# Kernel tuning notes

Measured on AMD Instinct MI355X. Metric: run time of the kernel, lower is better.

The kernel has to match this reference:

```python
import jax, jax.numpy as jnp
import numpy as np

N_NODES = 100000


def _gcn_norm(edge_index, num_nodes):
    # PyG GCNConv default: add self-loops, symmetric normalization
    src, dst = edge_index[0], edge_index[1]
    loop = jnp.arange(num_nodes, dtype=src.dtype)
    src = jnp.concatenate([src, loop])
    dst = jnp.concatenate([dst, loop])
    deg = jax.ops.segment_sum(jnp.ones_like(dst, dtype=jnp.float32), dst,
                              num_segments=num_nodes)
    dinv = jnp.where(deg > 0, jax.lax.rsqrt(deg), 0.0)
    norm = dinv[src] * dinv[dst]  # [E + N]
    return src, dst, norm


def _gcn_conv(x, W, b, src, dst, norm, num_nodes):
    h = x @ W                                   # [N, out] linear first (PyG)
    msg = h[src] * norm[:, None]                # gather + scale  [E+N, out]
    out = jax.ops.segment_sum(msg, dst, num_segments=num_nodes)  # scatter-add
    return out + b


def setup_inputs() -> dict:
    key = jax.random.key(0)
    ks = jax.random.split(key, 5)
    x = jax.random.normal(ks[0], (N_NODES, 3), dtype=jnp.float32)
    edge_index = jax.random.randint(ks[1], (2, 1600000), 0, N_NODES, dtype=jnp.int64)
    # Glorot-ish weights, zero bias (PyG defaults)
    W1 = jax.random.normal(ks[2], (3, 64), dtype=jnp.float32) * (1.0 / np.sqrt(3))
    W2 = jax.random.normal(ks[3], (64, 64), dtype=jnp.float32) * (1.0 / np.sqrt(64))
    W3 = jax.random.normal(ks[4], (64, 3), dtype=jnp.float32) * (1.0 / np.sqrt(64))
    b1 = jnp.zeros((64,), jnp.float32)
    b2 = jnp.zeros((64,), jnp.float32)
    b3 = jnp.zeros((3,), jnp.float32)
    return {"x": x, "edge_index": edge_index, "W1": W1, "b1": b1,
            "W2": W2, "b2": b2, "W3": W3, "b3": b3}


def reference(x, edge_index, W1, b1, W2, b2, W3, b3):
    n = x.shape[0]
    src, dst, norm = _gcn_norm(edge_index, n)  # same graph for every layer
    h = jax.nn.relu(_gcn_conv(x, W1, b1, src, dst, norm, n))
    h = jax.nn.relu(_gcn_conv(h, W2, b2, src, dst, norm, n))
    return _gcn_conv(h, W3, b3, src, dst, norm, n)
```

## Files before the change

### kernel.cpp

```cpp
#include <hip/hip_runtime.h>

#define TPB 256
#define NB 391
#define CH 4096
#define BS 4736


__device__ __forceinline__ unsigned bpack(float a, float b) {
    unsigned ua = __float_as_uint(a), ub = __float_as_uint(b);
    ua = (ua + 0x7fffu + ((ua >> 16) & 1u)) >> 16;
    ub = (ub + 0x7fffu + ((ub >> 16) & 1u)) >> 16;
    return ua | (ub << 16);
}
__device__ __forceinline__ float blo(unsigned u) { return __uint_as_float(u << 16); }
__device__ __forceinline__ float bhi(unsigned u) { return __uint_as_float(u & 0xffff0000u); }


__global__ __launch_bounds__(TPB) void k_placeA(const int* __restrict__ src,
                                                const int* __restrict__ dst,
                                                unsigned* __restrict__ gcur,
                                                unsigned* __restrict__ bkt, int E) {
    __shared__ unsigned val[CH];
    __shared__ unsigned dstS[CH];
    __shared__ unsigned short bid[CH];
    __shared__ unsigned cnt[512], loff[512], lcur[512], basev[512];
    __shared__ unsigned tsum[TPB];
    int t = threadIdx.x;
    int c0 = blockIdx.x * CH;
    int n = E - c0; if (n > CH) n = CH;

    for (int b = t; b < 512; b += TPB) { cnt[b] = 0; lcur[b] = 0; }
    __syncthreads();
    for (int i = t; i < n; i += TPB) {
        unsigned d = (unsigned)dst[c0 + i];
        dstS[i] = d;
        atomicAdd(&cnt[d >> 8], 1u);
    }
    __syncthreads();
    for (int b = t; b < NB; b += TPB)
        basev[b] = cnt[b] ? atomicAdd(&gcur[b], cnt[b]) : 0u;
    unsigned a0 = cnt[2 * t], a1 = cnt[2 * t + 1];
    tsum[t] = a0 + a1;
    __syncthreads();
#pragma unroll
    for (int o = 1; o < TPB; o <<= 1) {
        unsigned v = (t >= o) ? tsum[t - o] : 0u;
        __syncthreads();
        tsum[t] += v;
        __syncthreads();
    }
    unsigned ex = tsum[t] - (a0 + a1);
    loff[2 * t] = ex; loff[2 * t + 1] = ex + a0;
    __syncthreads();
    for (int i = t; i < n; i += TPB) {
        unsigned s = (unsigned)src[c0 + i];
        unsigned d = dstS[i];
        unsigned b = d >> 8;
        unsigned r = atomicAdd(&lcur[b], 1u);
        unsigned slot = loff[b] + r;
        val[slot] = s | ((d & 255u) << 20);
        bid[slot] = (unsigned short)b;
    }
    __syncthreads();
    for (int i = t; i < n; i += TPB) {
        unsigned b = bid[i];
        bkt[(size_t)b * BS + basev[b] + ((unsigned)i - loff[b])] = val[i];
    }
}


__global__ __launch_bounds__(512) void k_fineS(const unsigned* __restrict__ bkt,
                                               const unsigned* __restrict__ gcur,
                                               const float* __restrict__ x,
                                               int2* __restrict__ rp2,
                                               int* __restrict__ ssrc,
                                               float* __restrict__ dinv,
                                               float4* __restrict__ xs4, int N) {
    __shared__ unsigned bins[4096];
    __shared__ unsigned tsum[512];
    __shared__ unsigned degS[256];
    __shared__ unsigned bs[BS];
    int t = threadIdx.x, b = blockIdx.x;
    for (int i = t; i < 4096; i += 512) bins[i] = 0;
    __syncthreads();
    int p0 = b * BS;
    int n = (int)gcur[b];
    for (int i = t; i < n; i += 512) {
        unsigned u = bkt[p0 + i];
        bs[i] = u;
        unsigned bin = ((u >> 20) << 4) | ((u & 0xFFFFFu) >> 13);
        atomicAdd(&bins[bin], 1u);
    }
    __syncthreads();
    unsigned s[8], pre[8];
#pragma unroll
    for (int i = 0; i < 8; ++i) s[i] = bins[8 * t + i];
    if (t < 256) {
        unsigned d = 0;
#pragma unroll
        for (int i = 0; i < 16; ++i) d += bins[(t << 4) + i];
        degS[t] = d;
    }
    unsigned tot = 0;
#pragma unroll
    for (int i = 0; i < 8; ++i) { pre[i] = tot; tot += s[i]; }
    tsum[t] = tot;
    __syncthreads();
#pragma unroll
    for (int o = 1; o < 512; o <<= 1) {
        unsigned v = (t >= o) ? tsum[t - o] : 0u;
        __syncthreads();
        tsum[t] += v;
        __syncthreads();
    }
    unsigned ex = tsum[t] - tot;
#pragma unroll
    for (int i = 0; i < 8; ++i) bins[8 * t + i] = ex + pre[i];
    __syncthreads();
    if (t < 256) {
        int node = (b << 8) + t;
        if (node < N) {
            unsigned c = degS[t];
            int beg = p0 + (int)bins[t << 4];
            rp2[node] = make_int2(beg, beg + (int)c);
            float dv = rsqrtf((float)(c + 1u));
            dinv[node] = dv;
            float4 xv;
            xv.x = x[node * 3 + 0] * dv;
            xv.y = x[node * 3 + 1] * dv;
            xv.z = x[node * 3 + 2] * dv;
            xv.w = 0.f;
            xs4[node] = xv;
        }
    }
    __syncthreads();
    for (int i = t; i < n; i += 512) {
        unsigned u = bs[i];
        unsigned bin = ((u >> 20) << 4) | ((u & 0xFFFFFu) >> 13);
        unsigned r = atomicAdd(&bins[bin], 1u);
        ssrc[p0 + (int)r] = (int)(u & 0xFFFFFu);
    }
}


__global__ __launch_bounds__(TPB) void k_l1q(const float* __restrict__ xs4,
                                             const int2* __restrict__ rp2,
                                             const int* __restrict__ ssrc,
                                             const float* __restrict__ dinv,
                                             const float* __restrict__ W1,
                                             const float* __restrict__ b1,
                                             const float* __restrict__ W2,
                                             uint4* __restrict__ gb, int N) {
    __shared__ unsigned Ws2[2048];
    for (int i = threadIdx.x; i < 2048; i += TPB)
        Ws2[i] = bpack(W2[2 * i], W2[2 * i + 1]);
    __syncthreads();
    int tid = blockIdx.x * TPB + threadIdx.x;
    int node = tid >> 2, c = tid & 3;
    if (node >= N) return;
    int2 r = rp2[node];
    float acc = xs4[tid];
    int j = r.x;
    for (; j + 3 < r.y; j += 4) {
        int s0 = ssrc[j], s1 = ssrc[j+1], s2 = ssrc[j+2], s3 = ssrc[j+3];
        acc += (xs4[(s0 << 2) + c] + xs4[(s1 << 2) + c])
             + (xs4[(s2 << 2) + c] + xs4[(s3 << 2) + c]);
    }
    for (; j < r.y; ++j) acc += xs4[(ssrc[j] << 2) + c];
    float dv = dinv[node];
    acc *= dv;
    int base = (threadIdx.x & 63) & ~3;
    float q0 = __shfl(acc, base + 0, 64);
    float q1 = __shfl(acc, base + 1, 64);
    float q2 = __shfl(acc, base + 2, 64);

    float o[16];
#pragma unroll
    for (int i = 0; i < 16; ++i) o[i] = 0.f;
    const int cofs8 = c << 3;
    for (int kb = 0; kb < 16; ++kb) {
        int k0 = __builtin_amdgcn_readfirstlane(kb) << 2;
        const float* W1k = W1 + k0;
        const float* b1k = b1 + k0;
        float h[4];
        h[0] = fmaxf(fmaf(q0, W1k[0], fmaf(q1, W1k[64], fmaf(q2, W1k[128], b1k[0]))), 0.f);
        h[1] = fmaxf(fmaf(q0, W1k[1], fmaf(q1, W1k[65], fmaf(q2, W1k[129], b1k[1]))), 0.f);
        h[2] = fmaxf(fmaf(q0, W1k[2], fmaf(q1, W1k[66], fmaf(q2, W1k[130], b1k[2]))), 0.f);
        h[3] = fmaxf(fmaf(q0, W1k[3], fmaf(q1, W1k[67], fmaf(q2, W1k[131], b1k[3]))), 0.f);
#pragma unroll
        for (int kk = 0; kk < 4; ++kk) {
            const uint4* Wp = (const uint4*)(Ws2 + ((k0 + kk) << 5) + cofs8);
            uint4 wA = Wp[0];
            uint4 wB = Wp[1];
            float hv = h[kk];
            o[0]  = fmaf(hv, blo(wA.x), o[0]);  o[1]  = fmaf(hv, bhi(wA.x), o[1]);
            o[2]  = fmaf(hv, blo(wA.y), o[2]);  o[3]  = fmaf(hv, bhi(wA.y), o[3]);
            o[4]  = fmaf(hv, blo(wA.z), o[4]);  o[5]  = fmaf(hv, bhi(wA.z), o[5]);
            o[6]  = fmaf(hv, blo(wA.w), o[6]);  o[7]  = fmaf(hv, bhi(wA.w), o[7]);
            o[8]  = fmaf(hv, blo(wB.x), o[8]);  o[9]  = fmaf(hv, bhi(wB.x), o[9]);
            o[10] = fmaf(hv, blo(wB.y), o[10]); o[11] = fmaf(hv, bhi(wB.y), o[11]);
            o[12] = fmaf(hv, blo(wB.z), o[12]); o[13] = fmaf(hv, bhi(wB.z), o[13]);
            o[14] = fmaf(hv, blo(wB.w), o[14]); o[15] = fmaf(hv, bhi(wB.w), o[15]);
        }
    }
    uint4 v0, v1;
    v0.x = bpack(o[0] * dv,  o[1] * dv);
    v0.y = bpack(o[2] * dv,  o[3] * dv);
    v0.z = bpack(o[4] * dv,  o[5] * dv);
    v0.w = bpack(o[6] * dv,  o[7] * dv);
    v1.x = bpack(o[8] * dv,  o[9] * dv);
    v1.y = bpack(o[10] * dv, o[11] * dv);
    v1.z = bpack(o[12] * dv, o[13] * dv);
    v1.w = bpack(o[14] * dv, o[15] * dv);
    uint4* gp = gb + ((size_t)node << 3) + (c << 1);
    gp[0] = v0;
    gp[1] = v1;
}


__global__ __launch_bounds__(TPB) void k_p2fb(const uint4* __restrict__ gb,
                                              const int2* __restrict__ rp2,
                                              const int* __restrict__ ssrc,
                                              const float* __restrict__ dinv,
                                              const float* __restrict__ b2,
                                              const float* __restrict__ W3,
                                              float* __restrict__ q4, int N) {
    int tid = blockIdx.x * TPB + threadIdx.x;
    int node = tid >> 3, q = tid & 7;
    if (node >= N) return;
    int2 r = rp2[node];
    int beg = r.x, end = r.y;
    float a[8];
    {
        uint4 u = gb[((size_t)node << 3) + q];
        a[0] = blo(u.x); a[1] = bhi(u.x);
        a[2] = blo(u.y); a[3] = bhi(u.y);
        a[4] = blo(u.z); a[5] = bhi(u.z);
        a[6] = blo(u.w); a[7] = bhi(u.w);
    }
    int j = beg;
    for (; j + 3 < end; j += 4) {
        int s0 = ssrc[j], s1 = ssrc[j+1], s2 = ssrc[j+2], s3 = ssrc[j+3];
        uint4 u0 = gb[((size_t)s0 << 3) + q];
        uint4 u1 = gb[((size_t)s1 << 3) + q];
        uint4 u2 = gb[((size_t)s2 << 3) + q];
        uint4 u3 = gb[((size_t)s3 << 3) + q];
        a[0] += (blo(u0.x) + blo(u1.x)) + (blo(u2.x) + blo(u3.x));
        a[1] += (bhi(u0.x) + bhi(u1.x)) + (bhi(u2.x) + bhi(u3.x));
        a[2] += (blo(u0.y) + blo(u1.y)) + (blo(u2.y) + blo(u3.y));
        a[3] += (bhi(u0.y) + bhi(u1.y)) + (bhi(u2.y) + bhi(u3.y));
        a[4] += (blo(u0.z) + blo(u1.z)) + (blo(u2.z) + blo(u3.z));
        a[5] += (bhi(u0.z) + bhi(u1.z)) + (bhi(u2.z) + bhi(u3.z));
        a[6] += (blo(u0.w) + blo(u1.w)) + (blo(u2.w) + blo(u3.w));
        a[7] += (bhi(u0.w) + bhi(u1.w)) + (bhi(u2.w) + bhi(u3.w));
    }
    for (; j < end; ++j) {
        uint4 u = gb[((size_t)ssrc[j] << 3) + q];
        a[0] += blo(u.x); a[1] += bhi(u.x);
        a[2] += blo(u.y); a[3] += bhi(u.y);
        a[4] += blo(u.z); a[5] += bhi(u.z);
        a[6] += blo(u.w); a[7] += bhi(u.w);
    }
    float dv = dinv[node];
    int f0 = q << 3;
    const float* bb = b2 + f0;
    const float* Wr = W3 + f0 * 3;
    float p0 = 0.f, p1 = 0.f, p2 = 0.f;
#pragma unroll
    for (int i = 0; i < 8; ++i) {
        float h = fmaxf(fmaf(a[i], dv, bb[i]), 0.f);
        p0 = fmaf(h, Wr[3*i+0], p0);
        p1 = fmaf(h, Wr[3*i+1], p1);
        p2 = fmaf(h, Wr[3*i+2], p2);
    }
#pragma unroll
    for (int off = 1; off < 8; off <<= 1) {
        p0 += __shfl_xor(p0, off, 64);
        p1 += __shfl_xor(p1, off, 64);
        p2 += __shfl_xor(p2, off, 64);
    }
    if (q < 4) {
        float v = (q == 0) ? p0 * dv : (q == 1) ? p1 * dv : (q == 2) ? p2 * dv : 0.f;
        q4[((size_t)node << 2) + q] = v;
    }
}


__global__ __launch_bounds__(TPB) void k_pull3o(const float* __restrict__ g34,
                                                const int2* __restrict__ rp2,
                                                const int* __restrict__ ssrc,
                                                const float* __restrict__ dinv,
                                                const float* __restrict__ b3,
                                                float* __restrict__ out, int N) {
    int tid = blockIdx.x * TPB + threadIdx.x;
    int node = tid >> 2, c = tid & 3;
    if (node >= N) return;
    int2 r = rp2[node];
    int beg = r.x, end = r.y;
    float acc = g34[tid];
    int j = beg;
    for (; j + 3 < end; j += 4) {
        int s0 = ssrc[j], s1 = ssrc[j+1], s2 = ssrc[j+2], s3 = ssrc[j+3];
        acc += (g34[(s0 << 2) + c] + g34[(s1 << 2) + c])
             + (g34[(s2 << 2) + c] + g34[(s3 << 2) + c]);
    }
    for (; j < end; ++j) acc += g34[(ssrc[j] << 2) + c];
    if (c < 3) out[(size_t)node * 3 + c] = dinv[node] * acc + b3[c];
}

extern "C" void kernel_launch(void* const* d_in, const int* in_sizes, int n_in,
                              void* d_out, int out_size, void* d_ws, size_t ws_size,
                              hipStream_t stream) {
    const float* x  = (const float*)d_in[0];
    const int*   ei = (const int*)  d_in[1];
    const float* W1 = (const float*)d_in[2];
    const float* b1 = (const float*)d_in[3];
    const float* W2 = (const float*)d_in[4];
    const float* b2 = (const float*)d_in[5];
    const float* W3 = (const float*)d_in[6];
    const float* b3 = (const float*)d_in[7];
    float* out = (float*)d_out;

    const int N = in_sizes[0] / 3;
    const int E = in_sizes[1] / 2;
    const int* srcI = ei;
    const int* dstI = ei + E;

    float*    ws   = (float*)d_ws;
    unsigned* gcur = (unsigned*)ws;
    int2*     rp2  = (int2*)    (ws + 512);
    float*    dinv = ws + 512 + 2 * (size_t)N;
    int*      ssrc = (int*)     (dinv + N);
    float*    xs4  = (float*)(ssrc + (size_t)NB * BS + 4);
    float*    q4   = xs4 + (size_t)N * 4;
    unsigned* gb   = (unsigned*)(q4 + (size_t)N * 4);
    unsigned* bkt  = gb + (size_t)N * 32;

    int gPlace = (E + CH - 1) / CH;
    int gS3    = (N * 4 + TPB - 1) / TPB;
    int gP2    = (int)(((size_t)N * 8 + TPB - 1) / TPB);

    hipMemsetAsync(gcur, 0, 512 * sizeof(unsigned), stream);
    k_placeA<<<gPlace, TPB, 0, stream>>>(srcI, dstI, gcur, bkt, E);
    k_fineS <<<NB,     512, 0, stream>>>(bkt, gcur, x, rp2, ssrc, dinv,
                                         (float4*)xs4, N);

    k_l1q<<<gS3, TPB, 0, stream>>>(xs4, rp2, ssrc, dinv,
                                   W1, b1, W2, (uint4*)gb, N);

    k_p2fb<<<gP2, TPB, 0, stream>>>((const uint4*)gb, rp2, ssrc, dinv,
                                    b2, W3, q4, N);

    k_pull3o<<<gS3, TPB, 0, stream>>>(q4, rp2, ssrc, dinv, b3, out, N);
}
```

Before: 205.7 us.

## Sort nodes by degree so layer-1/2 warps process uniform neighbor counts

Builds a per-block degree histogram in k_fineS, scans it in a tiny kernel, and produces a degree-sorted node permutation via a new k_dperm kernel. Layers 1 and 2 then map threads to nodes through this permutation so that lanes in a wavefront have similar edge counts, reducing divergence and tail imbalance in the gather loops. The cost is two extra kernel launches, an extra indirection read per thread, and loss of locality in the node-indexed writes and self-feature reads. The workspace layout shifts to fit the histogram, cursors and permutation array.

```diff
diff --git a/kernel.cpp b/kernel.cpp
--- a/kernel.cpp
+++ b/kernel.cpp
@@ -75,13 +75,16 @@
                                                int2* __restrict__ rp2,
                                                int* __restrict__ ssrc,
                                                float* __restrict__ dinv,
-                                               float4* __restrict__ xs4, int N) {
+                                               float4* __restrict__ xs4,
+                                               unsigned* __restrict__ gdh, int N) {
     __shared__ unsigned bins[4096];
     __shared__ unsigned tsum[512];
     __shared__ unsigned degS[256];
+    __shared__ unsigned dh[64];
     __shared__ unsigned bs[BS];
     int t = threadIdx.x, b = blockIdx.x;
     for (int i = t; i < 4096; i += 512) bins[i] = 0;
+    if (t < 64) dh[t] = 0;
     __syncthreads();
     int p0 = b * BS;
     int n = (int)gcur[b];
@@ -121,6 +124,7 @@
         int node = (b << 8) + t;
         if (node < N) {
             unsigned c = degS[t];
+            atomicAdd(&dh[c < 63u ? c : 63u], 1u);
             int beg = p0 + (int)bins[t << 4];
             rp2[node] = make_int2(beg, beg + (int)c);
             float dv = rsqrtf((float)(c + 1u));
@@ -134,6 +138,7 @@
         }
     }
     __syncthreads();
+    if (t < 64 && dh[t]) atomicAdd(&gdh[t], dh[t]);
     for (int i = t; i < n; i += 512) {
         unsigned u = bs[i];
         unsigned bin = ((u >> 20) << 4) | ((u & 0xFFFFFu) >> 13);
@@ -143,10 +148,50 @@
 }
 
 
+__global__ __launch_bounds__(64) void k_dscan(const unsigned* __restrict__ gdh,
+                                              unsigned* __restrict__ dcur) {
+    int t = threadIdx.x;
+    unsigned v = gdh[t];
+    unsigned sum = v;
+#pragma unroll
+    for (int o = 1; o < 64; o <<= 1) {
+        unsigned u = __shfl_up(sum, o, 64);
+        if (t >= o) sum += u;
+    }
+    dcur[t] = sum - v;
+}
+
+
+__global__ __launch_bounds__(TPB) void k_dperm(const int2* __restrict__ rp2,
+                                               unsigned* __restrict__ dcur,
+                                               int* __restrict__ perm, int N) {
+    __shared__ unsigned dh[64], basev[64], lcur[64];
+    int t = threadIdx.x;
+    int node = blockIdx.x * TPB + t;
+    if (t < 64) { dh[t] = 0; lcur[t] = 0; }
+    __syncthreads();
+    int bin = -1;
+    if (node < N) {
+        int2 r = rp2[node];
+        unsigned d = (unsigned)(r.y - r.x);
+        bin = d < 63u ? (int)d : 63;
+        atomicAdd(&dh[bin], 1u);
+    }
+    __syncthreads();
+    if (t < 64) basev[t] = dh[t] ? atomicAdd(&dcur[t], dh[t]) : 0u;
+    __syncthreads();
+    if (node < N) {
+        unsigned rk = atomicAdd(&lcur[bin], 1u);
+        perm[basev[bin] + rk] = node;
+    }
+}
+
+
 __global__ __launch_bounds__(TPB) void k_l1q(const float* __restrict__ xs4,
                                              const int2* __restrict__ rp2,
                                              const int* __restrict__ ssrc,
                                              const float* __restrict__ dinv,
+                                             const int* __restrict__ perm,
                                              const float* __restrict__ W1,
                                              const float* __restrict__ b1,
                                              const float* __restrict__ W2,
@@ -156,10 +201,11 @@
         Ws2[i] = bpack(W2[2 * i], W2[2 * i + 1]);
     __syncthreads();
     int tid = blockIdx.x * TPB + threadIdx.x;
-    int node = tid >> 2, c = tid & 3;
-    if (node >= N) return;
+    int slot = tid >> 2, c = tid & 3;
+    if (slot >= N) return;
+    int node = perm[slot];
     int2 r = rp2[node];
-    float acc = xs4[tid];
+    float acc = xs4[(node << 2) + c];
     int j = r.x;
     for (; j + 3 < r.y; j += 4) {
         int s0 = ssrc[j], s1 = ssrc[j+1], s2 = ssrc[j+2], s3 = ssrc[j+3];
@@ -222,12 +268,14 @@
                                               const int2* __restrict__ rp2,
                                               const int* __restrict__ ssrc,
                                               const float* __restrict__ dinv,
+                                              const int* __restrict__ perm,
                                               const float* __restrict__ b2,
                                               const float* __restrict__ W3,
                                               float* __restrict__ q4, int N) {
     int tid = blockIdx.x * TPB + threadIdx.x;
-    int node = tid >> 3, q = tid & 7;
-    if (node >= N) return;
+    int slot = tid >> 3, q = tid & 7;
+    if (slot >= N) return;
+    int node = perm[slot];
     int2 r = rp2[node];
     int beg = r.x, end = r.y;
     float a[8];
@@ -328,10 +376,13 @@
 
     float*    ws   = (float*)d_ws;
     unsigned* gcur = (unsigned*)ws;
-    int2*     rp2  = (int2*)    (ws + 512);
-    float*    dinv = ws + 512 + 2 * (size_t)N;
+    unsigned* gdh  = (unsigned*)(ws + 512);
+    unsigned* dcur = (unsigned*)(ws + 576);
+    int*      perm = (int*)     (ws + 640);
+    int2*     rp2  = (int2*)    (ws + 640 + N);
+    float*    dinv = ws + 640 + 3 * (size_t)N;
     int*      ssrc = (int*)     (dinv + N);
-    float*    xs4  = (float*)(ssrc + (size_t)NB * BS + 4);
+    float*    xs4  = (float*)(ssrc + (size_t)NB * BS);
     float*    q4   = xs4 + (size_t)N * 4;
     unsigned* gb   = (unsigned*)(q4 + (size_t)N * 4);
     unsigned* bkt  = gb + (size_t)N * 32;
@@ -339,16 +390,19 @@
     int gPlace = (E + CH - 1) / CH;
     int gS3    = (N * 4 + TPB - 1) / TPB;
     int gP2    = (int)(((size_t)N * 8 + TPB - 1) / TPB);
-
-    hipMemsetAsync(gcur, 0, 512 * sizeof(unsigned), stream);
+    int gN     = (N + TPB - 1) / TPB;
+
+    hipMemsetAsync(gcur, 0, 576 * sizeof(unsigned), stream);
     k_placeA<<<gPlace, TPB, 0, stream>>>(srcI, dstI, gcur, bkt, E);
     k_fineS <<<NB,     512, 0, stream>>>(bkt, gcur, x, rp2, ssrc, dinv,
-                                         (float4*)xs4, N);
-
-    k_l1q<<<gS3, TPB, 0, stream>>>(xs4, rp2, ssrc, dinv,
+                                         (float4*)xs4, gdh, N);
+    k_dscan <<<1,       64, 0, stream>>>(gdh, dcur);
+    k_dperm <<<gN,     TPB, 0, stream>>>(rp2, dcur, perm, N);
+
+    k_l1q<<<gS3, TPB, 0, stream>>>(xs4, rp2, ssrc, dinv, perm,
                                    W1, b1, W2, (uint4*)gb, N);
 
-    k_p2fb<<<gP2, TPB, 0, stream>>>((const uint4*)gb, rp2, ssrc, dinv,
+    k_p2fb<<<gP2, TPB, 0, stream>>>((const uint4*)gb, rp2, ssrc, dinv, perm,
                                     b2, W3, q4, N);
 
     k_pull3o<<<gS3, TPB, 0, stream>>>(q4, rp2, ssrc, dinv, b3, out, N);
```

After: 206.2 us. About the same (+0.3%).
